# Kernel optimization log

Hardware: AMD Instinct MI355X
Metric: run time of the kernel (lower is better)

The kernel has to match this reference:

```python
import jax, jax.numpy as jnp
import numpy as np

DIM = 1024
N_HEADS = 16
HEAD_DIM = DIM // N_HEADS


def setup_inputs() -> dict:
    key = jax.random.key(0)
    ks = jax.random.split(key, 5)
    s = 1.0 / np.sqrt(DIM)
    return {
        "x": jax.random.normal(ks[0], (2, 2048, DIM), dtype=jnp.float32),
        "w_qkv": jax.random.normal(ks[1], (DIM, 3 * DIM), dtype=jnp.float32) * s,
        "b_qkv": jnp.zeros((3 * DIM,), dtype=jnp.float32),
        "w_proj": jax.random.normal(ks[2], (DIM, DIM), dtype=jnp.float32) * s,
        "b_proj": jnp.zeros((DIM,), dtype=jnp.float32),
    }


def reference(x, w_qkv, b_qkv, w_proj, b_proj):
    B, T, C = x.shape
    qkv = x @ w_qkv + b_qkv                      # [B,T,3C]
    qkv = qkv.reshape(B, T, 3, N_HEADS, HEAD_DIM)
    q, k, v = qkv[:, :, 0], qkv[:, :, 1], qkv[:, :, 2]  # [B,T,H,D]
    scale = 1.0 / np.sqrt(HEAD_DIM)
    scores = jnp.einsum("bqhd,bkhd->bhqk", q, k) * scale  # [B,H,T,T]
    attn = jax.nn.softmax(scores, axis=-1)
    out = jnp.einsum("bhqk,bkhd->bqhd", attn, v)          # [B,T,H,D]
    out = out.reshape(B, T, C)
    return out @ w_proj + b_proj
```

## Files before the change

### kernel.cpp

```cpp
#include <hip/hip_runtime.h>

typedef unsigned short u16;
typedef unsigned int   u32;
typedef __bf16 bf16x8 __attribute__((ext_vector_type(8)));
typedef float  f32x4  __attribute__((ext_vector_type(4)));
typedef float  f32x16 __attribute__((ext_vector_type(16)));

#define TSEQ 2048
#define NHEAD 16
#define HDIM 64
#define CDIM 1024
#define N3   3072
#define MROWS 4096

__device__ __forceinline__ u16 f2bf(float f) {
    union { float f; u32 u; } v; v.f = f;
    u32 r = v.u + 0x7FFFu + ((v.u >> 16) & 1u);
    return (u16)(r >> 16);
}

__device__ __forceinline__ u32 pkbf(float a, float b) {
#if __has_builtin(__builtin_amdgcn_cvt_pk_bf16_f32)
    typedef __bf16 bf16x2 __attribute__((ext_vector_type(2)));
    bf16x2 t = __builtin_amdgcn_cvt_pk_bf16_f32(a, b);
    union { bf16x2 v; u32 u; } c; c.v = t; return c.u;
#else
    union { float f; u32 u; } ua, ub; ua.f = a; ub.f = b;
    u32 sel = 0x07060302, d;
    asm("v_perm_b32 %0, %1, %2, %3" : "=v"(d) : "v"(ub.u), "v"(ua.u), "v"(sel));
    return d;
#endif
}

__device__ __forceinline__ void gld16(const u16* g, u16* l) {
    __builtin_amdgcn_global_load_lds(
        (const __attribute__((address_space(1))) u32*)g,
        (__attribute__((address_space(3))) u32*)l, 16, 0, 0);
}

__global__ __launch_bounds__(256) void prep_kernel(const float* __restrict__ x,
                                                   const float* __restrict__ wqkv,
                                                   const float* __restrict__ wproj,
                                                   u16* __restrict__ Xb,
                                                   u16* __restrict__ oqkv, u16* __restrict__ oproj) {
    __shared__ float tile[32][33];
    const int bx = blockIdx.x;
    const int tid = threadIdx.x;
    if (bx < 4096) {
        int i = bx * 256 + tid;
        float4 v = reinterpret_cast<const float4*>(x)[i];
        ushort4 o;
        o.x = f2bf(v.x); o.y = f2bf(v.y); o.z = f2bf(v.z); o.w = f2bf(v.w);
        reinterpret_cast<ushort4*>(Xb)[i] = o;
        return;
    }
    int idx = bx - 4096;
    int bnx = idx & 127;
    int k0  = (idx >> 7) * 32;
    const float* in; u16* out; int N, n0;
    if (bnx < 96) { in = wqkv;  out = oqkv;  N = 3072; n0 = bnx * 32; }
    else          { in = wproj; out = oproj; N = 1024; n0 = (bnx - 96) * 32; }
    int tx = tid & 31, ty = tid >> 5;
#pragma unroll
    for (int i = 0; i < 4; i++)
        tile[ty + i * 8][tx] = in[(size_t)(k0 + ty + i * 8) * N + n0 + tx];
    __syncthreads();
#pragma unroll
    for (int i = 0; i < 4; i++)
        out[(size_t)(n0 + ty + i * 8) * 1024 + k0 + tx] = f2bf(tile[tx][ty + i * 8]);
}

__global__ __launch_bounds__(256) void gemm_qkv(const u16* __restrict__ A, const u16* __restrict__ Bt,
                                                const float* __restrict__ bias, u16* __restrict__ Qf,
                                                u16* __restrict__ Kf, u16* __restrict__ Vf) {
    __shared__ __align__(16) u16 Al[128 * 32];
    __shared__ __align__(16) u16 Bl[128 * 32];
    __shared__ __align__(16) u16 Im[16384];
    const int tid  = threadIdx.x;
    const int lane = tid & 63;
    const int wave = tid >> 6;
    const int wm = (wave >> 1) * 64;
    const int wn = (wave & 1) * 64;
    const int row0 = blockIdx.x * 128;
    const int col0 = blockIdx.y * 128;
    const int lr = lane & 15;
    const int lq = lane >> 4;
    const float c2 = 0.125f * 1.44269504088896f;

    f32x4 acc[4][4];
#pragma unroll
    for (int i = 0; i < 4; i++)
#pragma unroll
        for (int j = 0; j < 4; j++) acc[i][j] = f32x4{0.f, 0.f, 0.f, 0.f};

    const int sr = tid >> 2, sc_ = (tid & 3) * 8;

    for (int k0 = 0; k0 < CDIM; k0 += 32) {
#pragma unroll
        for (int s = 0; s < 2; s++) {
            int i = tid + s * 256;
            int r = sr + s * 64;
            gld16(&A[(size_t)(row0 + r) * CDIM + k0 + sc_], &Al[i * 8]);
            gld16(&Bt[(size_t)(col0 + r) * CDIM + k0 + sc_], &Bl[i * 8]);
        }
        __syncthreads();
        bf16x8 af[4], bfr[4];
#pragma unroll
        for (int t = 0; t < 4; t++) {
            af[t]  = *reinterpret_cast<const bf16x8*>(&Al[(wm + t * 16 + lr) * 32 + lq * 8]);
            bfr[t] = *reinterpret_cast<const bf16x8*>(&Bl[(wn + t * 16 + lr) * 32 + lq * 8]);
        }
#pragma unroll
        for (int mt = 0; mt < 4; mt++)
#pragma unroll
            for (int nt = 0; nt < 4; nt++)
                acc[mt][nt] = __builtin_amdgcn_mfma_f32_16x16x32_bf16(af[mt], bfr[nt], acc[mt][nt], 0, 0, 0);
        __syncthreads();
    }

    const int region = col0 >> 10;
    const int h_base = (col0 & 1023) >> 6;
#pragma unroll
    for (int mt = 0; mt < 4; mt++) {
#pragma unroll
        for (int nt = 0; nt < 4; nt++) {
            int n_local = wn + nt * 16 + lr;
            float bv = bias[col0 + n_local];
            int h_local = n_local >> 6;
            int d = n_local & 63;
#pragma unroll
            for (int r = 0; r < 4; r++) {
                int m_local = wm + mt * 16 + lq * 4 + r;
                float v = acc[mt][nt][r] + bv;
                if (region == 0) {
                    int qt_local = m_local >> 5, q31 = m_local & 31;
                    int kc = d >> 4, l5b = (d >> 3) & 1, j = d & 7;
                    int lc = (h_local * 4 + qt_local) * 4 + kc;
                    Im[lc * 512 + (l5b * 32 + q31) * 8 + j] = f2bf(v * c2);
                } else if (region == 1) {
                    int kb_local = m_local >> 6, tr = m_local & 63;
                    int kc = d >> 4, l5b = (d >> 3) & 1, j = d & 7;
                    int nt2 = tr >> 5, p31 = tr & 31;
                    int lc = (h_local * 2 + kb_local) * 8 + kc * 2 + nt2;
                    Im[lc * 512 + (l5b * 32 + p31) * 8 + j] = f2bf(v);
                } else {
                    int kb_local = m_local >> 6, tr = m_local & 63;
                    int cV = tr >> 4, dt2 = d >> 5, p31 = d & 31;
                    int l5b = (tr >> 2) & 1;
                    int j = ((tr >> 3) & 1) * 4 + (tr & 3);
                    int lc = (h_local * 2 + kb_local) * 8 + cV * 2 + dt2;
                    Im[lc * 512 + (l5b * 32 + p31) * 8 + j] = f2bf(v);
                }
            }
        }
    }
    __syncthreads();
    const int bq = row0 >> 11;
    const int qrow0 = row0 & 2047;
#pragma unroll
    for (int s = 0; s < 8; s++) {
        int slot = s * 256 + tid;
        int lc = slot >> 6, li = slot & 63;
        uint4 data = *reinterpret_cast<const uint4*>(&Im[slot * 8]);
        if (region == 0) {
            int h_local = lc >> 4, qt_local = (lc >> 2) & 3, kc = lc & 3;
            size_t off = ((size_t)((bq * 16 + h_base + h_local) * 64 + (qrow0 >> 5) + qt_local) * 4 + kc) * 512
                       + li * 8;
            *reinterpret_cast<uint4*>(Qf + off) = data;
        } else {
            int h_local = lc >> 4, kb_local = (lc >> 3) & 1, cit = lc & 7;
            size_t off = (size_t)((bq * 16 + h_base + h_local) * 32 + (qrow0 >> 6) + kb_local) * 4096
                       + cit * 512 + li * 8;
            *reinterpret_cast<uint4*>((region == 1 ? Kf : Vf) + off) = data;
        }
    }
}

__global__ __launch_bounds__(256) void gemm_proj(const u16* __restrict__ A, const u16* __restrict__ Bt,
                                                 const float* __restrict__ bias, float* __restrict__ C) {
    __shared__ __align__(16) u16 Al[2 * 64 * 32];
    __shared__ __align__(16) u16 Bl[2 * 128 * 32];
    const int tid  = threadIdx.x;
    const int lane = tid & 63;
    const int wave = tid >> 6;
    const int wm = (wave >> 1) * 32;
    const int wn = (wave & 1) * 64;
    const int row0 = blockIdx.x * 64;
    const int col0 = blockIdx.y * 128;
    const int lr = lane & 15;
    const int lq = lane >> 4;

    f32x4 acc[2][4];
#pragma unroll
    for (int i = 0; i < 2; i++)
#pragma unroll
        for (int j = 0; j < 4; j++) acc[i][j] = f32x4{0.f, 0.f, 0.f, 0.f};

    for (int k0 = 0; k0 < CDIM; k0 += 64) {
#pragma unroll
        for (int s = 0; s < 2; s++) {
            int i = tid + s * 256;
            int kk = i >> 8, rr = (i >> 2) & 63, cc = i & 3;
            gld16(&A[(size_t)(row0 + rr) * CDIM + k0 + kk * 32 + cc * 8], &Al[i * 8]);
        }
#pragma unroll
        for (int s = 0; s < 4; s++) {
            int i = tid + s * 256;
            int kk = i >> 9, rr = (i >> 2) & 127, cc = i & 3;
            gld16(&Bt[(size_t)(col0 + rr) * CDIM + k0 + kk * 32 + cc * 8], &Bl[i * 8]);
        }
        __syncthreads();
#pragma unroll
        for (int kk = 0; kk < 2; kk++) {
            bf16x8 af[2], bfr[4];
#pragma unroll
            for (int t = 0; t < 2; t++)
                af[t] = *reinterpret_cast<const bf16x8*>(&Al[kk * 2048 + (wm + t * 16 + lr) * 32 + lq * 8]);
#pragma unroll
            for (int t = 0; t < 4; t++)
                bfr[t] = *reinterpret_cast<const bf16x8*>(&Bl[kk * 4096 + (wn + t * 16 + lr) * 32 + lq * 8]);
#pragma unroll
            for (int mt = 0; mt < 2; mt++)
#pragma unroll
                for (int nt = 0; nt < 4; nt++)
                    acc[mt][nt] = __builtin_amdgcn_mfma_f32_16x16x32_bf16(af[mt], bfr[nt], acc[mt][nt], 0, 0, 0);
        }
        __syncthreads();
    }
#pragma unroll
    for (int mt = 0; mt < 2; mt++) {
#pragma unroll
        for (int nt = 0; nt < 4; nt++) {
            int col = col0 + wn + nt * 16 + lr;
            float bv = bias[col];
#pragma unroll
            for (int r = 0; r < 4; r++) {
                int row = row0 + wm + mt * 16 + lq * 4 + r;
                C[(size_t)row * CDIM + col] = acc[mt][nt][r] + bv;
            }
        }
    }
}

__global__ __launch_bounds__(256, 1) void attn_kernel(const u16* __restrict__ Qf,
                                                      const u16* __restrict__ Kf,
                                                      const u16* __restrict__ Vf,
                                                      u16* __restrict__ AO) {
    const int id = blockIdx.x;
    const int bh = id & 31;
    const int qb = id >> 5;
    const int b = bh >> 4, h = bh & 15;
    const int tid = threadIdx.x, lane = tid & 63, wave = tid >> 6;
    const int l31 = lane & 31, l5 = lane >> 5;
    const int qt0 = qb * 8 + wave * 2;

    bf16x8 qa0[4], qa1[4];
    {
        const u16* qp = Qf + ((size_t)(bh * 64 + qt0) * 4) * 512 + lane * 8;
#pragma unroll
        for (int kc = 0; kc < 4; kc++) {
            qa0[kc] = *reinterpret_cast<const bf16x8*>(qp + kc * 512);
            qa1[kc] = *reinterpret_cast<const bf16x8*>(qp + 2048 + kc * 512);
        }
    }
    f32x16 o00, o01, o10, o11, zc;
#pragma unroll
    for (int i = 0; i < 16; i++) { o00[i] = 0.f; o01[i] = 0.f; o10[i] = 0.f; o11[i] = 0.f; zc[i] = 0.f; }
    float l0 = 0.f, l1 = 0.f;

    const u16* kcur = Kf + (size_t)bh * 32 * 4096 + lane * 8;
    const u16* vcur = Vf + (size_t)bh * 32 * 4096 + lane * 8;

    bf16x8 ka[8];
#pragma unroll
    for (int i = 0; i < 8; i++) ka[i] = *reinterpret_cast<const bf16x8*>(kcur + i * 512);

    for (int kb = 0; kb < 32; kb++) {
        f32x16 st00, st01, st10, st11;
        st00 = __builtin_amdgcn_mfma_f32_32x32x16_bf16(ka[0], qa0[0], zc, 0, 0, 0);
        st01 = __builtin_amdgcn_mfma_f32_32x32x16_bf16(ka[1], qa0[0], zc, 0, 0, 0);
        st10 = __builtin_amdgcn_mfma_f32_32x32x16_bf16(ka[0], qa1[0], zc, 0, 0, 0);
        st11 = __builtin_amdgcn_mfma_f32_32x32x16_bf16(ka[1], qa1[0], zc, 0, 0, 0);
#pragma unroll
        for (int kc = 1; kc < 4; kc++) {
            st00 = __builtin_amdgcn_mfma_f32_32x32x16_bf16(ka[kc * 2],     qa0[kc], st00, 0, 0, 0);
            st01 = __builtin_amdgcn_mfma_f32_32x32x16_bf16(ka[kc * 2 + 1], qa0[kc], st01, 0, 0, 0);
            st10 = __builtin_amdgcn_mfma_f32_32x32x16_bf16(ka[kc * 2],     qa1[kc], st10, 0, 0, 0);
            st11 = __builtin_amdgcn_mfma_f32_32x32x16_bf16(ka[kc * 2 + 1], qa1[kc], st11, 0, 0, 0);
        }
        bf16x8 vfr[8];
#pragma unroll
        for (int i = 0; i < 8; i++) vfr[i] = *reinterpret_cast<const bf16x8*>(vcur + i * 512);
        const u16* knext = kcur + (kb < 31 ? 4096 : 0);
#pragma unroll
        for (int i = 0; i < 8; i++) ka[i] = *reinterpret_cast<const bf16x8*>(knext + i * 512);
        kcur = knext;
        vcur += 4096;
        bf16x8 pa0[4], pa1[4];
        {
            float pe[16];
#pragma unroll
            for (int r = 0; r < 16; r++) { pe[r] = __builtin_amdgcn_exp2f(st00[r]); l0 += pe[r]; }
            union { bf16x8 v; u32 w[4]; } ua, ub;
#pragma unroll
            for (int j = 0; j < 4; j++) { ua.w[j] = pkbf(pe[2 * j], pe[2 * j + 1]); ub.w[j] = pkbf(pe[8 + 2 * j], pe[8 + 2 * j + 1]); }
            pa0[0] = ua.v; pa0[1] = ub.v;
#pragma unroll
            for (int r = 0; r < 16; r++) { pe[r] = __builtin_amdgcn_exp2f(st01[r]); l0 += pe[r]; }
#pragma unroll
            for (int j = 0; j < 4; j++) { ua.w[j] = pkbf(pe[2 * j], pe[2 * j + 1]); ub.w[j] = pkbf(pe[8 + 2 * j], pe[8 + 2 * j + 1]); }
            pa0[2] = ua.v; pa0[3] = ub.v;
#pragma unroll
            for (int r = 0; r < 16; r++) { pe[r] = __builtin_amdgcn_exp2f(st10[r]); l1 += pe[r]; }
#pragma unroll
            for (int j = 0; j < 4; j++) { ua.w[j] = pkbf(pe[2 * j], pe[2 * j + 1]); ub.w[j] = pkbf(pe[8 + 2 * j], pe[8 + 2 * j + 1]); }
            pa1[0] = ua.v; pa1[1] = ub.v;
#pragma unroll
            for (int r = 0; r < 16; r++) { pe[r] = __builtin_amdgcn_exp2f(st11[r]); l1 += pe[r]; }
#pragma unroll
            for (int j = 0; j < 4; j++) { ua.w[j] = pkbf(pe[2 * j], pe[2 * j + 1]); ub.w[j] = pkbf(pe[8 + 2 * j], pe[8 + 2 * j + 1]); }
            pa1[2] = ua.v; pa1[3] = ub.v;
        }
#pragma unroll
        for (int c = 0; c < 4; c++) {
            o00 = __builtin_amdgcn_mfma_f32_32x32x16_bf16(pa0[c], vfr[c * 2],     o00, 0, 0, 0);
            o01 = __builtin_amdgcn_mfma_f32_32x32x16_bf16(pa0[c], vfr[c * 2 + 1], o01, 0, 0, 0);
            o10 = __builtin_amdgcn_mfma_f32_32x32x16_bf16(pa1[c], vfr[c * 2],     o10, 0, 0, 0);
            o11 = __builtin_amdgcn_mfma_f32_32x32x16_bf16(pa1[c], vfr[c * 2 + 1], o11, 0, 0, 0);
        }
    }
    {
        float l = l0;
        l += __shfl_xor(l, 32);
        float linv = 1.0f / l;
        int q0 = qt0 * 32;
#pragma unroll
        for (int reg = 0; reg < 16; reg++) {
            int qrow = (reg & 3) + 8 * (reg >> 2) + 4 * l5;
            float li = __shfl(linv, qrow);
            AO[(size_t)(b * TSEQ + q0 + qrow) * CDIM + h * 64 + l31]      = f2bf(o00[reg] * li);
            AO[(size_t)(b * TSEQ + q0 + qrow) * CDIM + h * 64 + 32 + l31] = f2bf(o01[reg] * li);
        }
    }
    {
        float l = l1;
        l += __shfl_xor(l, 32);
        float linv = 1.0f / l;
        int q0 = (qt0 + 1) * 32;
#pragma unroll
        for (int reg = 0; reg < 16; reg++) {
            int qrow = (reg & 3) + 8 * (reg >> 2) + 4 * l5;
            float li = __shfl(linv, qrow);
            AO[(size_t)(b * TSEQ + q0 + qrow) * CDIM + h * 64 + l31]      = f2bf(o10[reg] * li);
            AO[(size_t)(b * TSEQ + q0 + qrow) * CDIM + h * 64 + 32 + l31] = f2bf(o11[reg] * li);
        }
    }
}

extern "C" void kernel_launch(void* const* d_in, const int* in_sizes, int n_in,
                              void* d_out, int out_size, void* d_ws, size_t ws_size,
                              hipStream_t stream) {
    const float* x      = (const float*)d_in[0];
    const float* w_qkv  = (const float*)d_in[1];
    const float* b_qkv  = (const float*)d_in[2];
    const float* w_proj = (const float*)d_in[3];
    const float* b_proj = (const float*)d_in[4];
    float* out = (float*)d_out;

    u16* ws     = (u16*)d_ws;
    u16* Xb     = ws;
    u16* Wqkvt  = Xb + 4194304;
    u16* Wprojt = Wqkvt + 3145728;
    u16* Qf     = Wprojt + 1048576;
    u16* Kf     = Qf + 4194304;
    u16* Vf     = Kf + 4194304;
    u16* AO     = Vf + 4194304;

    prep_kernel<<<8192, 256, 0, stream>>>(x, w_qkv, w_proj, Xb, Wqkvt, Wprojt);
    gemm_qkv<<<dim3(32, 24), 256, 0, stream>>>(Xb, Wqkvt, b_qkv, Qf, Kf, Vf);
    attn_kernel<<<256, 256, 0, stream>>>(Qf, Kf, Vf, AO);
    gemm_proj<<<dim3(64, 8), 256, 0, stream>>>(AO, Wprojt, b_proj, out);
}
```

Before: 173.6 us.

## Double-buffer LDS tiles in QKV and projection GEMMs to overlap loads

Both GEMM kernels now use two LDS buffers and issue the async global-to-LDS loads for the next K slice before computing on the current one, halving the number of barriers per K step. The QKV kernel reuses the epilogue staging buffer as the double-buffer storage, so LDS use shrinks. The projection kernel grows its LDS to hold two stages. This trades slightly higher LDS pressure in proj for hiding global load latency behind MFMA work.

```diff
diff --git a/kernel.cpp b/kernel.cpp
--- a/kernel.cpp
+++ b/kernel.cpp
@@ -70,12 +70,31 @@
         out[(size_t)(n0 + ty + i * 8) * 1024 + k0 + tx] = f2bf(tile[tx][ty + i * 8]);
 }
 
+#define QKV_STAGE(K0, AOFF, BOFF)                                                            \
+    _Pragma("unroll") for (int s = 0; s < 2; s++) {                                          \
+        int i = tid + s * 256;                                                               \
+        int r = sr + s * 64;                                                                 \
+        gld16(&A[(size_t)(row0 + r) * CDIM + (K0) + sc_], &smem[(AOFF) + i * 8]);            \
+        gld16(&Bt[(size_t)(col0 + r) * CDIM + (K0) + sc_], &smem[(BOFF) + i * 8]);           \
+    }
+
+#define QKV_COMPUTE(AOFF, BOFF)                                                              \
+    {                                                                                        \
+        bf16x8 af[4], bfr[4];                                                                \
+        _Pragma("unroll") for (int t = 0; t < 4; t++) {                                      \
+            af[t]  = *reinterpret_cast<const bf16x8*>(&smem[(AOFF) + (wm + t * 16 + lr) * 32 + lq * 8]); \
+            bfr[t] = *reinterpret_cast<const bf16x8*>(&smem[(BOFF) + (wn + t * 16 + lr) * 32 + lq * 8]); \
+        }                                                                                    \
+        _Pragma("unroll") for (int mt = 0; mt < 4; mt++)                                     \
+            _Pragma("unroll") for (int nt = 0; nt < 4; nt++)                                 \
+                acc[mt][nt] = __builtin_amdgcn_mfma_f32_16x16x32_bf16(af[mt], bfr[nt], acc[mt][nt], 0, 0, 0); \
+    }
+
 __global__ __launch_bounds__(256) void gemm_qkv(const u16* __restrict__ A, const u16* __restrict__ Bt,
                                                 const float* __restrict__ bias, u16* __restrict__ Qf,
                                                 u16* __restrict__ Kf, u16* __restrict__ Vf) {
-    __shared__ __align__(16) u16 Al[128 * 32];
-    __shared__ __align__(16) u16 Bl[128 * 32];
-    __shared__ __align__(16) u16 Im[16384];
+    __shared__ __align__(16) u16 smem[16384];
+    u16* Im = smem;
     const int tid  = threadIdx.x;
     const int lane = tid & 63;
     const int wave = tid >> 6;
@@ -95,28 +114,21 @@
 
     const int sr = tid >> 2, sc_ = (tid & 3) * 8;
 
-    for (int k0 = 0; k0 < CDIM; k0 += 32) {
-#pragma unroll
-        for (int s = 0; s < 2; s++) {
-            int i = tid + s * 256;
-            int r = sr + s * 64;
-            gld16(&A[(size_t)(row0 + r) * CDIM + k0 + sc_], &Al[i * 8]);
-            gld16(&Bt[(size_t)(col0 + r) * CDIM + k0 + sc_], &Bl[i * 8]);
-        }
+    QKV_STAGE(0, 0, 4096);
+    __syncthreads();
+    for (int k0 = 0; k0 < CDIM - 64; k0 += 64) {
+        QKV_STAGE(k0 + 32, 8192, 12288);
+        QKV_COMPUTE(0, 4096);
         __syncthreads();
-        bf16x8 af[4], bfr[4];
-#pragma unroll
-        for (int t = 0; t < 4; t++) {
-            af[t]  = *reinterpret_cast<const bf16x8*>(&Al[(wm + t * 16 + lr) * 32 + lq * 8]);
-            bfr[t] = *reinterpret_cast<const bf16x8*>(&Bl[(wn + t * 16 + lr) * 32 + lq * 8]);
-        }
-#pragma unroll
-        for (int mt = 0; mt < 4; mt++)
-#pragma unroll
-            for (int nt = 0; nt < 4; nt++)
-                acc[mt][nt] = __builtin_amdgcn_mfma_f32_16x16x32_bf16(af[mt], bfr[nt], acc[mt][nt], 0, 0, 0);
+        QKV_STAGE(k0 + 64, 0, 4096);
+        QKV_COMPUTE(8192, 12288);
         __syncthreads();
     }
+    QKV_STAGE(992, 8192, 12288);
+    QKV_COMPUTE(0, 4096);
+    __syncthreads();
+    QKV_COMPUTE(8192, 12288);
+    __syncthreads();
 
     const int region = col0 >> 10;
     const int h_base = (col0 & 1023) >> 6;
@@ -176,10 +188,33 @@
     }
 }
 
+#define PROJ_STAGE(K0, AOFF, BOFF)                                                           \
+    _Pragma("unroll") for (int s = 0; s < 2; s++) {                                          \
+        int i = tid + s * 256;                                                               \
+        int kk = i >> 8, rr = (i >> 2) & 63, cc = i & 3;                                     \
+        gld16(&A[(size_t)(row0 + rr) * CDIM + (K0) + kk * 32 + cc * 8], &smem[(AOFF) + i * 8]); \
+    }                                                                                        \
+    _Pragma("unroll") for (int s = 0; s < 4; s++) {                                          \
+        int i = tid + s * 256;                                                               \
+        int kk = i >> 9, rr = (i >> 2) & 127, cc = i & 3;                                    \
+        gld16(&Bt[(size_t)(col0 + rr) * CDIM + (K0) + kk * 32 + cc * 8], &smem[(BOFF) + i * 8]); \
+    }
+
+#define PROJ_COMPUTE(AOFF, BOFF)                                                             \
+    _Pragma("unroll") for (int kk = 0; kk < 2; kk++) {                                       \
+        bf16x8 af[2], bfr[4];                                                                \
+        _Pragma("unroll") for (int t = 0; t < 2; t++)                                        \
+            af[t] = *reinterpret_cast<const bf16x8*>(&smem[(AOFF) + kk * 2048 + (wm + t * 16 + lr) * 32 + lq * 8]); \
+        _Pragma("unroll") for (int t = 0; t < 4; t++)                                        \
+            bfr[t] = *reinterpret_cast<const bf16x8*>(&smem[(BOFF) + kk * 4096 + (wn + t * 16 + lr) * 32 + lq * 8]); \
+        _Pragma("unroll") for (int mt = 0; mt < 2; mt++)                                     \
+            _Pragma("unroll") for (int nt = 0; nt < 4; nt++)                                 \
+                acc[mt][nt] = __builtin_amdgcn_mfma_f32_16x16x32_bf16(af[mt], bfr[nt], acc[mt][nt], 0, 0, 0); \
+    }
+
 __global__ __launch_bounds__(256) void gemm_proj(const u16* __restrict__ A, const u16* __restrict__ Bt,
                                                  const float* __restrict__ bias, float* __restrict__ C) {
-    __shared__ __align__(16) u16 Al[2 * 64 * 32];
-    __shared__ __align__(16) u16 Bl[2 * 128 * 32];
+    __shared__ __align__(16) u16 smem[24576];
     const int tid  = threadIdx.x;
     const int lane = tid & 63;
     const int wave = tid >> 6;
@@ -196,37 +231,21 @@
 #pragma unroll
         for (int j = 0; j < 4; j++) acc[i][j] = f32x4{0.f, 0.f, 0.f, 0.f};
 
-    for (int k0 = 0; k0 < CDIM; k0 += 64) {
-#pragma unroll
-        for (int s = 0; s < 2; s++) {
-            int i = tid + s * 256;
-            int kk = i >> 8, rr = (i >> 2) & 63, cc = i & 3;
-            gld16(&A[(size_t)(row0 + rr) * CDIM + k0 + kk * 32 + cc * 8], &Al[i * 8]);
-        }
-#pragma unroll
-        for (int s = 0; s < 4; s++) {
-            int i = tid + s * 256;
-            int kk = i >> 9, rr = (i >> 2) & 127, cc = i & 3;
-            gld16(&Bt[(size_t)(col0 + rr) * CDIM + k0 + kk * 32 + cc * 8], &Bl[i * 8]);
-        }
+    PROJ_STAGE(0, 0, 4096);
+    __syncthreads();
+    for (int k0 = 0; k0 < CDIM - 128; k0 += 128) {
+        PROJ_STAGE(k0 + 64, 12288, 16384);
+        PROJ_COMPUTE(0, 4096);
         __syncthreads();
-#pragma unroll
-        for (int kk = 0; kk < 2; kk++) {
-            bf16x8 af[2], bfr[4];
-#pragma unroll
-            for (int t = 0; t < 2; t++)
-                af[t] = *reinterpret_cast<const bf16x8*>(&Al[kk * 2048 + (wm + t * 16 + lr) * 32 + lq * 8]);
-#pragma unroll
-            for (int t = 0; t < 4; t++)
-                bfr[t] = *reinterpret_cast<const bf16x8*>(&Bl[kk * 4096 + (wn + t * 16 + lr) * 32 + lq * 8]);
-#pragma unroll
-            for (int mt = 0; mt < 2; mt++)
-#pragma unroll
-                for (int nt = 0; nt < 4; nt++)
-                    acc[mt][nt] = __builtin_amdgcn_mfma_f32_16x16x32_bf16(af[mt], bfr[nt], acc[mt][nt], 0, 0, 0);
-        }
+        PROJ_STAGE(k0 + 128, 0, 4096);
+        PROJ_COMPUTE(12288, 16384);
         __syncthreads();
     }
+    PROJ_STAGE(960, 12288, 16384);
+    PROJ_COMPUTE(0, 4096);
+    __syncthreads();
+    PROJ_COMPUTE(12288, 16384);
+
 #pragma unroll
     for (int mt = 0; mt < 2; mt++) {
 #pragma unroll
```

After: 170.6 us, median of 2. No clear change (-1.7%).
